# Kernel tuning notes

Hardware: AMD Instinct MI355X
Metric: run time of the kernel (lower is better)

Reference implementation:

```python
import jax, jax.numpy as jnp
import numpy as np

NUM_SUBSPACES = 8
CODEBOOK_SIZE = 256
SUBSPACE_DIM = 96


def setup_inputs() -> dict:
    key = jax.random.key(0)
    k1, k2 = jax.random.split(key)
    embeddings = jax.random.normal(k1, (16, 4096, NUM_SUBSPACES * SUBSPACE_DIM), dtype=jnp.float32)
    codebooks = jax.random.normal(k2, (NUM_SUBSPACES, CODEBOOK_SIZE, SUBSPACE_DIM), dtype=jnp.float32)
    return {"embeddings": embeddings, "codebooks": codebooks}


def reference(embeddings, codebooks):
    # embeddings: [B, S, E] with E = M*d; codebooks: [M, K, d]
    B, S, E = embeddings.shape
    M, K, d = codebooks.shape
    # [N, M, d] -> [M, N, d] so each subspace is contiguous
    x = embeddings.reshape(B * S, M, d).transpose(1, 0, 2)
    x2 = jnp.sum(x * x, axis=-1, keepdims=True)              # [M, N, 1]
    c2 = jnp.sum(codebooks * codebooks, axis=-1)[:, None, :]  # [M, 1, K]
    xc = jnp.einsum('mnd,mkd->mnk', x, codebooks)             # [M, N, K]
    dist2 = x2 - 2.0 * xc + c2                                # [M, N, K]
    # argmin over codes (same result as cdist p=2 argmin since sqrt is monotone)
    idx = jnp.argmin(dist2, axis=-1)                          # [M, N]
    # gather nearest codewords per subspace
    quantized = codebooks[jnp.arange(M)[:, None], idx]        # [M, N, d]
    # reassemble: [N, M, d] -> [B, S, E]
    return quantized.transpose(1, 0, 2).reshape(B, S, E)
```

## Files before the change

kernel.cpp:

```cpp
#include <hip/hip_runtime.h>

typedef short   bf16x8 __attribute__((ext_vector_type(8)));
typedef unsigned short u16x8 __attribute__((ext_vector_type(8)));
typedef float   f32x16 __attribute__((ext_vector_type(16)));

constexpr int NSUB  = 8;
constexpr int NCODE = 256;
constexpr int SDIM  = 96;
constexpr int EMB   = NSUB * SDIM;
constexpr float C_SHIFT = 192.0f;
constexpr float THR = 0.02f;

constexpr int    CB_UNITS      = 8 * 6 * 2 * 64;
constexpr size_t WS_FRAG_BYTES = (size_t)NSUB * CB_UNITS * 16;
constexpr size_t WS_NEEDED     = WS_FRAG_BYTES + (size_t)NSUB * NCODE * 4;

__device__ __forceinline__ unsigned short f2bf(float v) {
    unsigned u = __builtin_bit_cast(unsigned, v);
    u = u + 0x7FFFu + ((u >> 16) & 1u);
    return (unsigned short)(u >> 16);
}
__device__ __forceinline__ float bf2f(unsigned short h) {
    unsigned u = ((unsigned)h) << 16;
    return __builtin_bit_cast(float, u);
}

__global__ __launch_bounds__(256) void pq_prep(const float* __restrict__ cb,
                                               unsigned short* __restrict__ wsf,
                                               float* __restrict__ wsc2)
{
    const int m   = (int)blockIdx.x;
    const int tid = (int)threadIdx.x;
    {
        const float* c = cb + ((size_t)m * NCODE + tid) * SDIM;
        double s = 0.0;
        for (int k = 0; k < SDIM; ++k) { double v = (double)c[k]; s += v * v; }
        wsc2[m * NCODE + tid] = (float)(0.5 * s + (double)C_SHIFT);
    }
    for (int i = 0; i < 24; ++i) {
        int u  = i * 256 + tid;
        int l  = u & 63;
        int c6 = u >> 6;
        int h  = c6 & 1; c6 >>= 1;
        int s  = c6 % 6;
        int t  = c6 / 6;
        int code = t * 32 + (l & 31);
        int k0   = s * 16 + (l >> 5) * 8;
        const float* src = cb + (size_t)m * NCODE * SDIM + (size_t)code * SDIM + k0;
        u16x8 o;
        #pragma unroll
        for (int j = 0; j < 8; ++j) {
            float v = -src[j];
            unsigned short hb = f2bf(v);
            o[j] = (h == 0) ? hb : f2bf(v - bf2f(hb));
        }
        *(u16x8*)(wsf + ((size_t)m * CB_UNITS + u) * 8) = o;
    }
}

__global__ __launch_bounds__(128, 3) void pq_mfma15(
    const float* __restrict__ emb,
    const float* __restrict__ cb,
    const unsigned short* __restrict__ wsf,
    const float* __restrict__ wsc2,
    float* __restrict__ out,
    int nrows,
    int rowblks)
{
    const int tid  = (int)threadIdx.x;
    const int lane = tid & 63;
    const int hib  = lane >> 5;
    const int m    = (int)blockIdx.x & 7;
    const int rb   = ((int)blockIdx.x >> 3) * 2 + (tid >> 6);
    if (rb >= rowblks) return;
    const int row0 = rb * 32;

    const unsigned short* wb = wsf + (size_t)m * CB_UNITS * 8;
    const float* c2p = wsc2 + m * NCODE;

    bf16x8 xh[6], xl[6];
    {
        int r = row0 + (lane & 31);
        if (r >= nrows) r = nrows - 1;
        const float* xr = emb + (size_t)r * EMB + m * SDIM + hib * 8;
        #pragma unroll
        for (int s = 0; s < 6; ++s) {
            float4 v0 = *(const float4*)(xr + s * 16);
            float4 v1 = *(const float4*)(xr + s * 16 + 4);
            float v[8] = { v0.x, v0.y, v0.z, v0.w, v1.x, v1.y, v1.z, v1.w };
            #pragma unroll
            for (int j = 0; j < 8; ++j) {
                unsigned short hb = f2bf(v[j]);
                xh[s][j] = (short)hb;
                xl[s][j] = (short)f2bf(v[j] - bf2f(hb));
            }
        }
    }

    float b1 = 3.4e38f, b2 = 3.4e38f;
    int   i1 = 1 << 30, i2 = 1 << 30;
    #pragma unroll 1
    for (int p = 0; p < 4; ++p) {
        const int t0 = p * 2, t1 = t0 + 1;
        f32x16 a0, a1;
        #pragma unroll
        for (int rq = 0; rq < 4; ++rq) {
            float4 q0 = *(const float4*)(c2p + t0 * 32 + rq * 8 + hib * 4);
            float4 q1 = *(const float4*)(c2p + t1 * 32 + rq * 8 + hib * 4);
            a0[rq*4+0]=q0.x; a0[rq*4+1]=q0.y; a0[rq*4+2]=q0.z; a0[rq*4+3]=q0.w;
            a1[rq*4+0]=q1.x; a1[rq*4+1]=q1.y; a1[rq*4+2]=q1.z; a1[rq*4+3]=q1.w;
        }
        __builtin_amdgcn_s_setprio(1);
        #pragma unroll
        for (int s = 0; s < 6; ++s) {
            bf16x8 ah0 = *(const bf16x8*)(wb + (size_t)((((t0 * 6 + s) * 2) + 0) * 64 + lane) * 8);
            bf16x8 al0 = *(const bf16x8*)(wb + (size_t)((((t0 * 6 + s) * 2) + 1) * 64 + lane) * 8);
            bf16x8 ah1 = *(const bf16x8*)(wb + (size_t)((((t1 * 6 + s) * 2) + 0) * 64 + lane) * 8);
            bf16x8 al1 = *(const bf16x8*)(wb + (size_t)((((t1 * 6 + s) * 2) + 1) * 64 + lane) * 8);
            a0 = __builtin_amdgcn_mfma_f32_32x32x16_bf16(ah0, xh[s], a0, 0, 0, 0);
            a1 = __builtin_amdgcn_mfma_f32_32x32x16_bf16(ah1, xh[s], a1, 0, 0, 0);
            a0 = __builtin_amdgcn_mfma_f32_32x32x16_bf16(al0, xh[s], a0, 0, 0, 0);
            a1 = __builtin_amdgcn_mfma_f32_32x32x16_bf16(al1, xh[s], a1, 0, 0, 0);
            a0 = __builtin_amdgcn_mfma_f32_32x32x16_bf16(ah0, xl[s], a0, 0, 0, 0);
            a1 = __builtin_amdgcn_mfma_f32_32x32x16_bf16(ah1, xl[s], a1, 0, 0, 0);
        }
        __builtin_amdgcn_s_setprio(0);
        #pragma unroll
        for (int r = 0; r < 16; ++r) {
            float sv = a0[r];
            int   kv = t0 * 32 + (r & 3) + 8 * (r >> 2) + hib * 4;
            if (sv < b1)      { b2 = b1; i2 = i1; b1 = sv; i1 = kv; }
            else if (sv < b2) { b2 = sv; i2 = kv; }
        }
        #pragma unroll
        for (int r = 0; r < 16; ++r) {
            float sv = a1[r];
            int   kv = t1 * 32 + (r & 3) + 8 * (r >> 2) + hib * 4;
            if (sv < b1)      { b2 = b1; i2 = i1; b1 = sv; i1 = kv; }
            else if (sv < b2) { b2 = sv; i2 = kv; }
        }
    }
    {
        float ob1 = __shfl_xor(b1, 32);
        int   oi1 = __shfl_xor(i1, 32);
        float ob2 = __shfl_xor(b2, 32);
        int   oi2 = __shfl_xor(i2, 32);
        bool o1_better = (ob1 < b1) || (ob1 == b1 && oi1 < i1);
        if (o1_better) {
            bool mine_better = (b1 < ob2) || (b1 == ob2 && i1 < oi2);
            if (mine_better) { b2 = b1; i2 = i1; } else { b2 = ob2; i2 = oi2; }
            b1 = ob1; i1 = oi1;
        } else {
            if ((ob1 < b2) || (ob1 == b2 && oi1 < i2)) { b2 = ob1; i2 = oi1; }
        }
    }

    {
        int grow = row0 + (lane & 31);
        if (lane < 32 && grow < nrows && (b2 - b1 < THR)) {
            const float* xr = emb + (size_t)grow * EMB + m * SDIM;
            const float* ca = cb + ((size_t)m * NCODE + i1) * SDIM;
            const float* cbv = cb + ((size_t)m * NCODE + i2) * SDIM;
            double da = 0.0, db = 0.0;
            for (int kk = 0; kk < SDIM; ++kk) {
                double ea = (double)xr[kk] - (double)ca[kk];
                double eb = (double)xr[kk] - (double)cbv[kk];
                da += ea * ea; db += eb * eb;
            }
            if (db < da || (db == da && i2 < i1)) i1 = i2;
        }
    }

    #pragma unroll
    for (int ii = 0; ii < 12; ++ii) {
        int Q = ii * 64 + lane;
        int r = Q / 24, f = Q % 24;
        int grow = row0 + r;
        int k = __shfl(i1, r);
        if (grow < nrows) {
            float4 v = *(const float4*)(cb + ((size_t)m * NCODE + k) * SDIM + f * 4);
            *(float4*)(out + (size_t)grow * EMB + m * SDIM + f * 4) = v;
        }
    }
}

__global__ __launch_bounds__(256) void pq_argmin_kernel(
    const float* __restrict__ emb, const float* __restrict__ cb,
    float* __restrict__ out, int nrows)
{
    const int m   = (int)(blockIdx.x & 7);
    const int row = (int)(blockIdx.x >> 3) * 256 + (int)threadIdx.x;
    const float* __restrict__ cbm = cb + (size_t)m * (NCODE * SDIM);
    __shared__ float half_c2[NCODE];
    {
        const int k = (int)threadIdx.x;
        const float* c = cbm + k * SDIM;
        float s = 0.f;
        #pragma unroll
        for (int i = 0; i < SDIM; i += 4) {
            const float4 v = *reinterpret_cast<const float4*>(c + i);
            s = fmaf(v.x, v.x, s); s = fmaf(v.y, v.y, s);
            s = fmaf(v.z, v.z, s); s = fmaf(v.w, v.w, s);
        }
        half_c2[k] = 0.5f * s;
    }
    __syncthreads();
    if (row >= nrows) return;
    float x[SDIM];
    {
        const float* xr = emb + (size_t)row * EMB + m * SDIM;
        #pragma unroll
        for (int i = 0; i < SDIM; i += 4) {
            const float4 v = *reinterpret_cast<const float4*>(xr + i);
            x[i+0] = v.x; x[i+1] = v.y; x[i+2] = v.z; x[i+3] = v.w;
        }
    }
    float best = 3.4e38f, best2 = 3.4e38f;
    int bestk = 0, bestk2 = 0;
    #pragma unroll 1
    for (int k = 0; k < NCODE; k += 4) {
        const float* c0 = cbm + (k + 0) * SDIM;
        const float* c1 = cbm + (k + 1) * SDIM;
        const float* c2 = cbm + (k + 2) * SDIM;
        const float* c3 = cbm + (k + 3) * SDIM;
        float a0 = 0.f, a1 = 0.f, a2 = 0.f, a3 = 0.f;
        #pragma unroll
        for (int i = 0; i < SDIM; i += 4) {
            const float4 v0 = *reinterpret_cast<const float4*>(c0 + i);
            const float4 v1 = *reinterpret_cast<const float4*>(c1 + i);
            const float4 v2 = *reinterpret_cast<const float4*>(c2 + i);
            const float4 v3 = *reinterpret_cast<const float4*>(c3 + i);
            a0 = fmaf(x[i+0], v0.x, a0); a0 = fmaf(x[i+1], v0.y, a0);
            a0 = fmaf(x[i+2], v0.z, a0); a0 = fmaf(x[i+3], v0.w, a0);
            a1 = fmaf(x[i+0], v1.x, a1); a1 = fmaf(x[i+1], v1.y, a1);
            a1 = fmaf(x[i+2], v1.z, a1); a1 = fmaf(x[i+3], v1.w, a1);
            a2 = fmaf(x[i+0], v2.x, a2); a2 = fmaf(x[i+1], v2.y, a2);
            a2 = fmaf(x[i+2], v2.z, a2); a2 = fmaf(x[i+3], v2.w, a2);
            a3 = fmaf(x[i+0], v3.x, a3); a3 = fmaf(x[i+1], v3.y, a3);
            a3 = fmaf(x[i+2], v3.z, a3); a3 = fmaf(x[i+3], v3.w, a3);
        }
        const float s[4] = { half_c2[k+0] - a0, half_c2[k+1] - a1,
                             half_c2[k+2] - a2, half_c2[k+3] - a3 };
        #pragma unroll
        for (int j = 0; j < 4; ++j) {
            if (s[j] < best)       { best2 = best; bestk2 = bestk; best = s[j]; bestk = k + j; }
            else if (s[j] < best2) { best2 = s[j]; bestk2 = k + j; }
        }
    }
    if (best2 - best < 0.02f) {
        const float* ca = cbm + bestk  * SDIM;
        const float* cbv = cbm + bestk2 * SDIM;
        double da = 0.0, db = 0.0;
        for (int i = 0; i < SDIM; ++i) {
            const double ea = (double)x[i] - (double)ca[i];
            const double eb = (double)x[i] - (double)cbv[i];
            da += ea * ea; db += eb * eb;
        }
        if (db < da || (db == da && bestk2 < bestk)) bestk = bestk2;
    }
    const float* cbest = cbm + bestk * SDIM;
    float* o = out + (size_t)row * EMB + m * SDIM;
    #pragma unroll
    for (int i = 0; i < SDIM; i += 4)
        *reinterpret_cast<float4*>(o + i) = *reinterpret_cast<const float4*>(cbest + i);
}

extern "C" void kernel_launch(void* const* d_in, const int* in_sizes, int n_in,
                              void* d_out, int out_size, void* d_ws, size_t ws_size,
                              hipStream_t stream) {
    const float* emb = (const float*)d_in[0];
    const float* cb  = (const float*)d_in[1];
    float* out = (float*)d_out;
    const int nrows = in_sizes[0] / EMB;

    if (ws_size < WS_NEEDED) {
        const int rowBlocks = (nrows + 255) / 256;
        pq_argmin_kernel<<<dim3(rowBlocks * NSUB), dim3(256), 0, stream>>>(emb, cb, out, nrows);
        return;
    }

    unsigned short* wsf = (unsigned short*)d_ws;
    float* wsc2 = (float*)((char*)d_ws + WS_FRAG_BYTES);

    pq_prep<<<dim3(NSUB), dim3(256), 0, stream>>>(cb, wsf, wsc2);

    const int rowblks = (nrows + 31) / 32;
    const int nb      = ((rowblks + 1) / 2) * NSUB;
    pq_mfma15<<<dim3(nb), dim3(128), 0, stream>>>(emb, cb, wsf, wsc2, out, nrows, rowblks);
}
```

Baseline: 201.4 us.

## Switch to 16x16x32 MFMA tiles with 16-row blocks per wave

Replaces the 32x32x16 bf16 MFMA path with 16x16x32 MFMAs. Each wave now handles 16 rows instead of 32 and loops over 16 code tiles of 16 codes each. The codebook fragment prep layout is rebuilt to match, and an extra shuffle stage is added to merge the top-2 candidates across the four lane groups. This cuts per-wave register use and raises the number of blocks, but each wave now streams the whole codebook for half as many rows, so codebook reuse per load drops.

```diff
diff --git a/kernel.cpp b/kernel.cpp
--- a/kernel.cpp
+++ b/kernel.cpp
@@ -2,7 +2,7 @@
 
 typedef short   bf16x8 __attribute__((ext_vector_type(8)));
 typedef unsigned short u16x8 __attribute__((ext_vector_type(8)));
-typedef float   f32x16 __attribute__((ext_vector_type(16)));
+typedef float   f32x4  __attribute__((ext_vector_type(4)));
 
 constexpr int NSUB  = 8;
 constexpr int NCODE = 256;
@@ -11,8 +11,8 @@
 constexpr float C_SHIFT = 192.0f;
 constexpr float THR = 0.02f;
 
-constexpr int    CB_UNITS      = 8 * 6 * 2 * 64;
-constexpr size_t WS_FRAG_BYTES = (size_t)NSUB * CB_UNITS * 16;
+constexpr int    CB_UNITS16    = 16 * 3 * 2;
+constexpr size_t WS_FRAG_BYTES = (size_t)NSUB * CB_UNITS16 * 64 * 16;
 constexpr size_t WS_NEEDED     = WS_FRAG_BYTES + (size_t)NSUB * NCODE * 4;
 
 __device__ __forceinline__ unsigned short f2bf(float v) {
@@ -25,9 +25,21 @@
     return __builtin_bit_cast(float, u);
 }
 
-__global__ __launch_bounds__(256) void pq_prep(const float* __restrict__ cb,
-                                               unsigned short* __restrict__ wsf,
-                                               float* __restrict__ wsc2)
+__device__ __forceinline__ void merge_top2(float& b1, int& i1, float& b2, int& i2,
+                                           float ob1, int oi1, float ob2, int oi2) {
+    bool o1_better = (ob1 < b1) || (ob1 == b1 && oi1 < i1);
+    if (o1_better) {
+        bool mine_better = (b1 < ob2) || (b1 == ob2 && i1 < oi2);
+        if (mine_better) { b2 = b1; i2 = i1; } else { b2 = ob2; i2 = oi2; }
+        b1 = ob1; i1 = oi1;
+    } else {
+        if ((ob1 < b2) || (ob1 == b2 && oi1 < i2)) { b2 = ob1; i2 = oi1; }
+    }
+}
+
+__global__ __launch_bounds__(256) void pq_prep16(const float* __restrict__ cb,
+                                                 unsigned short* __restrict__ wsf,
+                                                 float* __restrict__ wsc2)
 {
     const int m   = (int)blockIdx.x;
     const int tid = (int)threadIdx.x;
@@ -38,14 +50,15 @@
         wsc2[m * NCODE + tid] = (float)(0.5 * s + (double)C_SHIFT);
     }
     for (int i = 0; i < 24; ++i) {
-        int u  = i * 256 + tid;
-        int l  = u & 63;
-        int c6 = u >> 6;
-        int h  = c6 & 1; c6 >>= 1;
-        int s  = c6 % 6;
-        int t  = c6 / 6;
-        int code = t * 32 + (l & 31);
-        int k0   = s * 16 + (l >> 5) * 8;
+        int idx = i * 256 + tid;
+        int l   = idx & 63;
+        int u   = idx >> 6;
+        int h   = u & 1;
+        int c6  = u >> 1;
+        int ks  = c6 % 3;
+        int t   = c6 / 3;
+        int code = t * 16 + (l & 15);
+        int k0   = ks * 32 + (l >> 4) * 8;
         const float* src = cb + (size_t)m * NCODE * SDIM + (size_t)code * SDIM + k0;
         u16x8 o;
         #pragma unroll
@@ -54,11 +67,11 @@
             unsigned short hb = f2bf(v);
             o[j] = (h == 0) ? hb : f2bf(v - bf2f(hb));
         }
-        *(u16x8*)(wsf + ((size_t)m * CB_UNITS + u) * 8) = o;
-    }
-}
-
-__global__ __launch_bounds__(128, 3) void pq_mfma15(
+        *(u16x8*)(wsf + ((size_t)m * 6144 + idx) * 8) = o;
+    }
+}
+
+__global__ __launch_bounds__(128) void pq_mfma16(
     const float* __restrict__ emb,
     const float* __restrict__ cb,
     const unsigned short* __restrict__ wsf,
@@ -69,30 +82,30 @@
 {
     const int tid  = (int)threadIdx.x;
     const int lane = tid & 63;
-    const int hib  = lane >> 5;
+    const int g4   = lane >> 4;
     const int m    = (int)blockIdx.x & 7;
     const int rb   = ((int)blockIdx.x >> 3) * 2 + (tid >> 6);
     if (rb >= rowblks) return;
-    const int row0 = rb * 32;
-
-    const unsigned short* wb = wsf + (size_t)m * CB_UNITS * 8;
+    const int row0 = rb * 16;
+
+    const unsigned short* wb = wsf + (size_t)m * 6144 * 8;
     const float* c2p = wsc2 + m * NCODE;
 
-    bf16x8 xh[6], xl[6];
-    {
-        int r = row0 + (lane & 31);
+    bf16x8 xh[3], xl[3];
+    {
+        int r = row0 + (lane & 15);
         if (r >= nrows) r = nrows - 1;
-        const float* xr = emb + (size_t)r * EMB + m * SDIM + hib * 8;
-        #pragma unroll
-        for (int s = 0; s < 6; ++s) {
-            float4 v0 = *(const float4*)(xr + s * 16);
-            float4 v1 = *(const float4*)(xr + s * 16 + 4);
+        const float* xr = emb + (size_t)r * EMB + m * SDIM + g4 * 8;
+        #pragma unroll
+        for (int ks = 0; ks < 3; ++ks) {
+            float4 v0 = *(const float4*)(xr + ks * 32);
+            float4 v1 = *(const float4*)(xr + ks * 32 + 4);
             float v[8] = { v0.x, v0.y, v0.z, v0.w, v1.x, v1.y, v1.z, v1.w };
             #pragma unroll
             for (int j = 0; j < 8; ++j) {
                 unsigned short hb = f2bf(v[j]);
-                xh[s][j] = (short)hb;
-                xl[s][j] = (short)f2bf(v[j] - bf2f(hb));
+                xh[ks][j] = (short)hb;
+                xl[ks][j] = (short)f2bf(v[j] - bf2f(hb));
             }
         }
     }
@@ -100,64 +113,49 @@
     float b1 = 3.4e38f, b2 = 3.4e38f;
     int   i1 = 1 << 30, i2 = 1 << 30;
     #pragma unroll 1
-    for (int p = 0; p < 4; ++p) {
-        const int t0 = p * 2, t1 = t0 + 1;
-        f32x16 a0, a1;
-        #pragma unroll
-        for (int rq = 0; rq < 4; ++rq) {
-            float4 q0 = *(const float4*)(c2p + t0 * 32 + rq * 8 + hib * 4);
-            float4 q1 = *(const float4*)(c2p + t1 * 32 + rq * 8 + hib * 4);
-            a0[rq*4+0]=q0.x; a0[rq*4+1]=q0.y; a0[rq*4+2]=q0.z; a0[rq*4+3]=q0.w;
-            a1[rq*4+0]=q1.x; a1[rq*4+1]=q1.y; a1[rq*4+2]=q1.z; a1[rq*4+3]=q1.w;
-        }
-        __builtin_amdgcn_s_setprio(1);
-        #pragma unroll
-        for (int s = 0; s < 6; ++s) {
-            bf16x8 ah0 = *(const bf16x8*)(wb + (size_t)((((t0 * 6 + s) * 2) + 0) * 64 + lane) * 8);
-            bf16x8 al0 = *(const bf16x8*)(wb + (size_t)((((t0 * 6 + s) * 2) + 1) * 64 + lane) * 8);
-            bf16x8 ah1 = *(const bf16x8*)(wb + (size_t)((((t1 * 6 + s) * 2) + 0) * 64 + lane) * 8);
-            bf16x8 al1 = *(const bf16x8*)(wb + (size_t)((((t1 * 6 + s) * 2) + 1) * 64 + lane) * 8);
-            a0 = __builtin_amdgcn_mfma_f32_32x32x16_bf16(ah0, xh[s], a0, 0, 0, 0);
-            a1 = __builtin_amdgcn_mfma_f32_32x32x16_bf16(ah1, xh[s], a1, 0, 0, 0);
-            a0 = __builtin_amdgcn_mfma_f32_32x32x16_bf16(al0, xh[s], a0, 0, 0, 0);
-            a1 = __builtin_amdgcn_mfma_f32_32x32x16_bf16(al1, xh[s], a1, 0, 0, 0);
-            a0 = __builtin_amdgcn_mfma_f32_32x32x16_bf16(ah0, xl[s], a0, 0, 0, 0);
-            a1 = __builtin_amdgcn_mfma_f32_32x32x16_bf16(ah1, xl[s], a1, 0, 0, 0);
-        }
-        __builtin_amdgcn_s_setprio(0);
-        #pragma unroll
-        for (int r = 0; r < 16; ++r) {
-            float sv = a0[r];
-            int   kv = t0 * 32 + (r & 3) + 8 * (r >> 2) + hib * 4;
+    for (int t = 0; t < 16; ++t) {
+        f32x4 a;
+        {
+            float4 q = *(const float4*)(c2p + t * 16 + g4 * 4);
+            a[0] = q.x; a[1] = q.y; a[2] = q.z; a[3] = q.w;
+        }
+        const unsigned short* tb = wb + t * 3072 + lane * 8;
+        #pragma unroll
+        for (int ks = 0; ks < 3; ++ks) {
+            bf16x8 ah = *(const bf16x8*)(tb + ks * 1024);
+            bf16x8 al = *(const bf16x8*)(tb + ks * 1024 + 512);
+            a = __builtin_amdgcn_mfma_f32_16x16x32_bf16(ah, xh[ks], a, 0, 0, 0);
+            a = __builtin_amdgcn_mfma_f32_16x16x32_bf16(al, xh[ks], a, 0, 0, 0);
+            a = __builtin_amdgcn_mfma_f32_16x16x32_bf16(ah, xl[ks], a, 0, 0, 0);
+            __builtin_amdgcn_sched_barrier(0);
+        }
+        const int kb = t * 16 + g4 * 4;
+        #pragma unroll
+        for (int r = 0; r < 4; ++r) {
+            float sv = a[r];
+            int   kv = kb + r;
             if (sv < b1)      { b2 = b1; i2 = i1; b1 = sv; i1 = kv; }
             else if (sv < b2) { b2 = sv; i2 = kv; }
         }
-        #pragma unroll
-        for (int r = 0; r < 16; ++r) {
-            float sv = a1[r];
-            int   kv = t1 * 32 + (r & 3) + 8 * (r >> 2) + hib * 4;
-            if (sv < b1)      { b2 = b1; i2 = i1; b1 = sv; i1 = kv; }
-            else if (sv < b2) { b2 = sv; i2 = kv; }
-        }
+    }
+    {
+        float ob1 = __shfl_xor(b1, 16);
+        int   oi1 = __shfl_xor(i1, 16);
+        float ob2 = __shfl_xor(b2, 16);
+        int   oi2 = __shfl_xor(i2, 16);
+        merge_top2(b1, i1, b2, i2, ob1, oi1, ob2, oi2);
     }
     {
         float ob1 = __shfl_xor(b1, 32);
         int   oi1 = __shfl_xor(i1, 32);
         float ob2 = __shfl_xor(b2, 32);
         int   oi2 = __shfl_xor(i2, 32);
-        bool o1_better = (ob1 < b1) || (ob1 == b1 && oi1 < i1);
-        if (o1_better) {
-            bool mine_better = (b1 < ob2) || (b1 == ob2 && i1 < oi2);
-            if (mine_better) { b2 = b1; i2 = i1; } else { b2 = ob2; i2 = oi2; }
-            b1 = ob1; i1 = oi1;
-        } else {
-            if ((ob1 < b2) || (ob1 == b2 && oi1 < i2)) { b2 = ob1; i2 = oi1; }
-        }
-    }
-
-    {
-        int grow = row0 + (lane & 31);
-        if (lane < 32 && grow < nrows && (b2 - b1 < THR)) {
+        merge_top2(b1, i1, b2, i2, ob1, oi1, ob2, oi2);
+    }
+
+    {
+        int grow = row0 + (lane & 15);
+        if (lane < 16 && grow < nrows && (b2 - b1 < THR)) {
             const float* xr = emb + (size_t)grow * EMB + m * SDIM;
             const float* ca = cb + ((size_t)m * NCODE + i1) * SDIM;
             const float* cbv = cb + ((size_t)m * NCODE + i2) * SDIM;
@@ -172,7 +170,7 @@
     }
 
     #pragma unroll
-    for (int ii = 0; ii < 12; ++ii) {
+    for (int ii = 0; ii < 6; ++ii) {
         int Q = ii * 64 + lane;
         int r = Q / 24, f = Q % 24;
         int grow = row0 + r;
@@ -282,9 +280,9 @@
     unsigned short* wsf = (unsigned short*)d_ws;
     float* wsc2 = (float*)((char*)d_ws + WS_FRAG_BYTES);
 
-    pq_prep<<<dim3(NSUB), dim3(256), 0, stream>>>(cb, wsf, wsc2);
-
-    const int rowblks = (nrows + 31) / 32;
+    pq_prep16<<<dim3(NSUB), dim3(256), 0, stream>>>(cb, wsf, wsc2);
+
+    const int rowblks = (nrows + 15) / 16;
     const int nb      = ((rowblks + 1) / 2) * NSUB;
-    pq_mfma15<<<dim3(nb), dim3(128), 0, stream>>>(emb, cb, wsf, wsc2, out, nrows, rowblks);
-}
+    pq_mfma16<<<dim3(nb), dim3(128), 0, stream>>>(emb, cb, wsf, wsc2, out, nrows, rowblks);
+}
```

New measurement: 234.4 us. 16.4% more time.

## Replace split-bf16 triple MFMA with single fp16 MFMA plus top-3 fp64 refinement

Applied to the files above, without the earlier changes.

Drops the hi/lo bf16 split of the codebook and embeddings (three MFMAs per step) in favor of one fp16 MFMA per step, and halves the prepared codebook fragment buffer. To recover the accuracy lost to fp16, the kernel now tracks the top-3 candidates, widens the near-tie threshold, and re-scores up to three candidates in double precision. This cuts MFMA work and fragment loads to about a third, at the cost of more registers and more rows taking the exact fallback path. The occupancy hint in launch bounds is also removed.

```diff
diff --git a/kernel.cpp b/kernel.cpp
--- a/kernel.cpp
+++ b/kernel.cpp
@@ -1,6 +1,6 @@
 #include <hip/hip_runtime.h>
 
-typedef short   bf16x8 __attribute__((ext_vector_type(8)));
+typedef _Float16 h8 __attribute__((ext_vector_type(8)));
 typedef unsigned short u16x8 __attribute__((ext_vector_type(8)));
 typedef float   f32x16 __attribute__((ext_vector_type(16)));
 
@@ -9,10 +9,9 @@
 constexpr int SDIM  = 96;
 constexpr int EMB   = NSUB * SDIM;
 constexpr float C_SHIFT = 192.0f;
-constexpr float THR = 0.02f;
-
-constexpr int    CB_UNITS      = 8 * 6 * 2 * 64;
-constexpr size_t WS_FRAG_BYTES = (size_t)NSUB * CB_UNITS * 16;
+constexpr float THR = 0.04f;
+
+constexpr size_t WS_FRAG_BYTES = (size_t)NSUB * 3072 * 16;
 constexpr size_t WS_NEEDED     = WS_FRAG_BYTES + (size_t)NSUB * NCODE * 4;
 
 __device__ __forceinline__ unsigned short f2bf(float v) {
@@ -20,14 +19,10 @@
     u = u + 0x7FFFu + ((u >> 16) & 1u);
     return (unsigned short)(u >> 16);
 }
-__device__ __forceinline__ float bf2f(unsigned short h) {
-    unsigned u = ((unsigned)h) << 16;
-    return __builtin_bit_cast(float, u);
-}
-
-__global__ __launch_bounds__(256) void pq_prep(const float* __restrict__ cb,
-                                               unsigned short* __restrict__ wsf,
-                                               float* __restrict__ wsc2)
+
+__global__ __launch_bounds__(256) void pq_prep_h(const float* __restrict__ cb,
+                                                 unsigned short* __restrict__ wsf,
+                                                 float* __restrict__ wsc2)
 {
     const int m   = (int)blockIdx.x;
     const int tid = (int)threadIdx.x;
@@ -37,28 +32,26 @@
         for (int k = 0; k < SDIM; ++k) { double v = (double)c[k]; s += v * v; }
         wsc2[m * NCODE + tid] = (float)(0.5 * s + (double)C_SHIFT);
     }
-    for (int i = 0; i < 24; ++i) {
-        int u  = i * 256 + tid;
-        int l  = u & 63;
-        int c6 = u >> 6;
-        int h  = c6 & 1; c6 >>= 1;
-        int s  = c6 % 6;
-        int t  = c6 / 6;
+    for (int i = 0; i < 12; ++i) {
+        int idx = i * 256 + tid;
+        int l   = idx & 63;
+        int u   = idx >> 6;
+        int s   = u % 6;
+        int t   = u / 6;
         int code = t * 32 + (l & 31);
         int k0   = s * 16 + (l >> 5) * 8;
         const float* src = cb + (size_t)m * NCODE * SDIM + (size_t)code * SDIM + k0;
         u16x8 o;
         #pragma unroll
         for (int j = 0; j < 8; ++j) {
-            float v = -src[j];
-            unsigned short hb = f2bf(v);
-            o[j] = (h == 0) ? hb : f2bf(v - bf2f(hb));
-        }
-        *(u16x8*)(wsf + ((size_t)m * CB_UNITS + u) * 8) = o;
-    }
-}
-
-__global__ __launch_bounds__(128, 3) void pq_mfma15(
+            _Float16 hv = (_Float16)(-src[j]);
+            o[j] = __builtin_bit_cast(unsigned short, hv);
+        }
+        *(u16x8*)(wsf + ((size_t)m * 3072 + idx) * 8) = o;
+    }
+}
+
+__global__ __launch_bounds__(128) void pq_mfma17(
     const float* __restrict__ emb,
     const float* __restrict__ cb,
     const unsigned short* __restrict__ wsf,
@@ -75,10 +68,10 @@
     if (rb >= rowblks) return;
     const int row0 = rb * 32;
 
-    const unsigned short* wb = wsf + (size_t)m * CB_UNITS * 8;
+    const unsigned short* wb = wsf + (size_t)m * 3072 * 8;
     const float* c2p = wsc2 + m * NCODE;
 
-    bf16x8 xh[6], xl[6];
+    h8 xh[6];
     {
         int r = row0 + (lane & 31);
         if (r >= nrows) r = nrows - 1;
@@ -89,16 +82,12 @@
             float4 v1 = *(const float4*)(xr + s * 16 + 4);
             float v[8] = { v0.x, v0.y, v0.z, v0.w, v1.x, v1.y, v1.z, v1.w };
             #pragma unroll
-            for (int j = 0; j < 8; ++j) {
-                unsigned short hb = f2bf(v[j]);
-                xh[s][j] = (short)hb;
-                xl[s][j] = (short)f2bf(v[j] - bf2f(hb));
-            }
-        }
-    }
-
-    float b1 = 3.4e38f, b2 = 3.4e38f;
-    int   i1 = 1 << 30, i2 = 1 << 30;
+            for (int j = 0; j < 8; ++j) xh[s][j] = (_Float16)v[j];
+        }
+    }
+
+    float b1 = 3.4e38f, b2 = 3.4e38f, b3 = 3.4e38f;
+    int   i1 = 1 << 30,  i2 = 1 << 30,  i3 = 1 << 30;
     #pragma unroll 1
     for (int p = 0; p < 4; ++p) {
         const int t0 = p * 2, t1 = t0 + 1;
@@ -113,61 +102,60 @@
         __builtin_amdgcn_s_setprio(1);
         #pragma unroll
         for (int s = 0; s < 6; ++s) {
-            bf16x8 ah0 = *(const bf16x8*)(wb + (size_t)((((t0 * 6 + s) * 2) + 0) * 64 + lane) * 8);
-            bf16x8 al0 = *(const bf16x8*)(wb + (size_t)((((t0 * 6 + s) * 2) + 1) * 64 + lane) * 8);
-            bf16x8 ah1 = *(const bf16x8*)(wb + (size_t)((((t1 * 6 + s) * 2) + 0) * 64 + lane) * 8);
-            bf16x8 al1 = *(const bf16x8*)(wb + (size_t)((((t1 * 6 + s) * 2) + 1) * 64 + lane) * 8);
-            a0 = __builtin_amdgcn_mfma_f32_32x32x16_bf16(ah0, xh[s], a0, 0, 0, 0);
-            a1 = __builtin_amdgcn_mfma_f32_32x32x16_bf16(ah1, xh[s], a1, 0, 0, 0);
-            a0 = __builtin_amdgcn_mfma_f32_32x32x16_bf16(al0, xh[s], a0, 0, 0, 0);
-            a1 = __builtin_amdgcn_mfma_f32_32x32x16_bf16(al1, xh[s], a1, 0, 0, 0);
-            a0 = __builtin_amdgcn_mfma_f32_32x32x16_bf16(ah0, xl[s], a0, 0, 0, 0);
-            a1 = __builtin_amdgcn_mfma_f32_32x32x16_bf16(ah1, xl[s], a1, 0, 0, 0);
+            h8 c0 = *(const h8*)(wb + (size_t)((t0 * 6 + s) * 64 + lane) * 8);
+            h8 c1 = *(const h8*)(wb + (size_t)((t1 * 6 + s) * 64 + lane) * 8);
+            a0 = __builtin_amdgcn_mfma_f32_32x32x16_f16(c0, xh[s], a0, 0, 0, 0);
+            a1 = __builtin_amdgcn_mfma_f32_32x32x16_f16(c1, xh[s], a1, 0, 0, 0);
         }
         __builtin_amdgcn_s_setprio(0);
         #pragma unroll
         for (int r = 0; r < 16; ++r) {
             float sv = a0[r];
             int   kv = t0 * 32 + (r & 3) + 8 * (r >> 2) + hib * 4;
-            if (sv < b1)      { b2 = b1; i2 = i1; b1 = sv; i1 = kv; }
-            else if (sv < b2) { b2 = sv; i2 = kv; }
+            if (sv < b1)      { b3 = b2; i3 = i2; b2 = b1; i2 = i1; b1 = sv; i1 = kv; }
+            else if (sv < b2) { b3 = b2; i3 = i2; b2 = sv; i2 = kv; }
+            else if (sv < b3) { b3 = sv; i3 = kv; }
         }
         #pragma unroll
         for (int r = 0; r < 16; ++r) {
             float sv = a1[r];
             int   kv = t1 * 32 + (r & 3) + 8 * (r >> 2) + hib * 4;
-            if (sv < b1)      { b2 = b1; i2 = i1; b1 = sv; i1 = kv; }
-            else if (sv < b2) { b2 = sv; i2 = kv; }
-        }
-    }
-    {
-        float ob1 = __shfl_xor(b1, 32);
-        int   oi1 = __shfl_xor(i1, 32);
-        float ob2 = __shfl_xor(b2, 32);
-        int   oi2 = __shfl_xor(i2, 32);
-        bool o1_better = (ob1 < b1) || (ob1 == b1 && oi1 < i1);
-        if (o1_better) {
-            bool mine_better = (b1 < ob2) || (b1 == ob2 && i1 < oi2);
-            if (mine_better) { b2 = b1; i2 = i1; } else { b2 = ob2; i2 = oi2; }
-            b1 = ob1; i1 = oi1;
-        } else {
-            if ((ob1 < b2) || (ob1 == b2 && oi1 < i2)) { b2 = ob1; i2 = oi1; }
-        }
+            if (sv < b1)      { b3 = b2; i3 = i2; b2 = b1; i2 = i1; b1 = sv; i1 = kv; }
+            else if (sv < b2) { b3 = b2; i3 = i2; b2 = sv; i2 = kv; }
+            else if (sv < b3) { b3 = sv; i3 = kv; }
+        }
+    }
+    {
+        float ob1 = __shfl_xor(b1, 32), ob2 = __shfl_xor(b2, 32), ob3 = __shfl_xor(b3, 32);
+        int   oi1 = __shfl_xor(i1, 32), oi2 = __shfl_xor(i2, 32), oi3 = __shfl_xor(i3, 32);
+        auto ins = [&](float s, int i) {
+            if (s < b1 || (s == b1 && i < i1))      { b3 = b2; i3 = i2; b2 = b1; i2 = i1; b1 = s; i1 = i; }
+            else if (s < b2 || (s == b2 && i < i2)) { b3 = b2; i3 = i2; b2 = s; i2 = i; }
+            else if (s < b3 || (s == b3 && i < i3)) { b3 = s; i3 = i; }
+        };
+        ins(ob1, oi1); ins(ob2, oi2); ins(ob3, oi3);
     }
 
     {
         int grow = row0 + (lane & 31);
         if (lane < 32 && grow < nrows && (b2 - b1 < THR)) {
+            int i3e = (b3 - b1 < THR) ? i3 : i1;
             const float* xr = emb + (size_t)grow * EMB + m * SDIM;
-            const float* ca = cb + ((size_t)m * NCODE + i1) * SDIM;
-            const float* cbv = cb + ((size_t)m * NCODE + i2) * SDIM;
-            double da = 0.0, db = 0.0;
+            const float* p1 = cb + ((size_t)m * NCODE + i1)  * SDIM;
+            const float* p2 = cb + ((size_t)m * NCODE + i2)  * SDIM;
+            const float* p3 = cb + ((size_t)m * NCODE + i3e) * SDIM;
+            double d1 = 0.0, d2 = 0.0, d3 = 0.0;
             for (int kk = 0; kk < SDIM; ++kk) {
-                double ea = (double)xr[kk] - (double)ca[kk];
-                double eb = (double)xr[kk] - (double)cbv[kk];
-                da += ea * ea; db += eb * eb;
+                double xv = (double)xr[kk];
+                double e1 = xv - (double)p1[kk];
+                double e2 = xv - (double)p2[kk];
+                double e3 = xv - (double)p3[kk];
+                d1 += e1 * e1; d2 += e2 * e2; d3 += e3 * e3;
             }
-            if (db < da || (db == da && i2 < i1)) i1 = i2;
+            double bd = d1; int bi = i1;
+            if (d2 < bd || (d2 == bd && i2  < bi)) { bd = d2; bi = i2; }
+            if (d3 < bd || (d3 == bd && i3e < bi)) { bd = d3; bi = i3e; }
+            i1 = bi;
         }
     }
 
@@ -282,9 +270,9 @@
     unsigned short* wsf = (unsigned short*)d_ws;
     float* wsc2 = (float*)((char*)d_ws + WS_FRAG_BYTES);
 
-    pq_prep<<<dim3(NSUB), dim3(256), 0, stream>>>(cb, wsf, wsc2);
+    pq_prep_h<<<dim3(NSUB), dim3(256), 0, stream>>>(cb, wsf, wsc2);
 
     const int rowblks = (nrows + 31) / 32;
     const int nb      = ((rowblks + 1) / 2) * NSUB;
-    pq_mfma15<<<dim3(nb), dim3(128), 0, stream>>>(emb, cb, wsf, wsc2, out, nrows, rowblks);
-}
+    pq_mfma17<<<dim3(nb), dim3(128), 0, stream>>>(emb, cb, wsf, wsc2, out, nrows, rowblks);
+}
```

Result: faster. 194.5 us (-3.4%).
